# Kernel tuning notes

Hardware: AMD Instinct MI355X
Metric: run time of the kernel (lower is better)

Reference implementation:

```python
import jax, jax.numpy as jnp
import numpy as np

D = 256        # emb_dim
H = 16         # num_heads
HD = D // H    # head_dim
N = 16384      # num users
B, S = 64, 128 # seq batch / length; M = B*S


def setup_inputs() -> dict:
    key = jax.random.key(0)
    ks = jax.random.split(key, 8)
    scale = 1.0 / np.sqrt(D)
    return {
        "user_feat": jax.random.normal(ks[0], (N, D), dtype=jnp.float32),
        "seq_feat": jax.random.normal(ks[1], (B, S, D), dtype=jnp.float32),
        "in_proj_w": jax.random.uniform(ks[2], (3 * D, D), jnp.float32, -scale, scale),
        "in_proj_b": jnp.zeros((3 * D,), jnp.float32),
        "out_proj_w": jax.random.uniform(ks[3], (D, D), jnp.float32, -scale, scale),
        "out_proj_b": jnp.zeros((D,), jnp.float32),
        "trans_w": jax.random.uniform(ks[4], (D, D), jnp.float32, -scale, scale),
        "trans_b": jax.random.uniform(ks[5], (D,), jnp.float32, -scale, scale),
    }


def _mha(x, in_proj_w, in_proj_b, out_proj_w, out_proj_b):
    # x: [B, S, D] self-attention, batch_first, like nn.MultiheadAttention
    qkv = jnp.einsum("bsd,ed->bse", x, in_proj_w) + in_proj_b  # [B,S,3D]
    q, k, v = jnp.split(qkv, 3, axis=-1)
    def heads(t):  # [B,S,D] -> [B,H,S,HD]
        return t.reshape(B, S, H, HD).transpose(0, 2, 1, 3)
    q, k, v = heads(q), heads(k), heads(v)
    scores = jnp.einsum("bhqd,bhkd->bhqk", q, k) / np.sqrt(HD)
    attn = jax.nn.softmax(scores, axis=-1)
    out = jnp.einsum("bhqk,bhkd->bhqd", attn, v)  # [B,H,S,HD]
    out = out.transpose(0, 2, 1, 3).reshape(B, S, D)
    return out @ out_proj_w.T + out_proj_b


def reference(user_feat, seq_feat, in_proj_w, in_proj_b, out_proj_w, out_proj_b, trans_w, trans_b):
    seq = _mha(seq_feat, in_proj_w, in_proj_b, out_proj_w, out_proj_b)
    seq = seq.reshape(-1, D)                        # [M, D]
    M = seq.shape[0]
    att = user_feat @ seq.T                         # [N, M]
    att = att / jnp.maximum(jnp.sum(jnp.abs(att), axis=1, keepdims=True), 1e-12)  # F.normalize p=1
    # mean_j Linear(att_ij * seq_j) == Linear((att @ seq) / M)  (exact, by linearity)
    agg = (att @ seq) / M                           # [N, D]
    return user_feat + (agg @ trans_w.T + trans_b)
```

## Files before the change

kernel.cpp:

```cpp
#include <hip/hip_runtime.h>


typedef __bf16 bf16_t;
typedef __bf16 bf16x8 __attribute__((ext_vector_type(8)));
typedef __bf16 bf16x4 __attribute__((ext_vector_type(4)));
typedef float  f32x4  __attribute__((ext_vector_type(4)));
typedef unsigned int u32x4 __attribute__((ext_vector_type(4)));

#define MFMA16(a, b, c) __builtin_amdgcn_mfma_f32_16x16x32_bf16((a), (b), (c), 0, 0, 0)

#define AS1 __attribute__((address_space(1)))
#define AS3 __attribute__((address_space(3)))
#define GLOAD_LDS16(g, l) \
    __builtin_amdgcn_global_load_lds((const AS1 unsigned int*)(const void*)(g), \
                                     (AS3 unsigned int*)(void*)(l), 16, 0, 0)

__device__ __forceinline__ int swz256(int row, int k) { return row * 256 + (k ^ ((row & 7) << 3)); }

__global__ void k_cvt(const float* __restrict__ s, bf16_t* __restrict__ d, int n4) {
    int i  = blockIdx.x * blockDim.x + threadIdx.x;
    int st = gridDim.x * blockDim.x;
    for (; i < n4; i += st) {
        float4 v = ((const float4*)s)[i];
        bf16x4 o = { (bf16_t)v.x, (bf16_t)v.y, (bf16_t)v.z, (bf16_t)v.w };
        ((bf16x4*)d)[i] = o;
    }
}

__global__ __launch_bounds__(256, 1)
void k_gemm_bt(const bf16_t* __restrict__ A, const bf16_t* __restrict__ B,
               const float* __restrict__ bias, bf16_t* __restrict__ Cb, int N) {
    __shared__ bf16_t Al[64 * 256];
    __shared__ bf16_t Bl[64 * 256];
    const int tid  = threadIdx.x;
    const int lane = tid & 63;
    const int w    = tid >> 6;
    const int l15  = lane & 15;
    const int l4   = lane >> 4;
    const int rb = blockIdx.y * 64, cb = blockIdx.x * 64;

    {
        const u32x4* sa = (const u32x4*)(A + (size_t)rb * 256);
        const u32x4* sb = (const u32x4*)(B + (size_t)cb * 256);
        u32x4* da = (u32x4*)Al;
        u32x4* db = (u32x4*)Bl;
#pragma unroll
        for (int i = 0; i < 8; ++i) {
            int ch  = i * 256 + tid;
            int row = ch >> 5, cp = ch & 31;
            int sch = (ch & ~31) | (cp ^ (row & 7));
            da[sch] = sa[ch];
            db[sch] = sb[ch];
        }
    }
    __syncthreads();

    f32x4 acc[4];
#pragma unroll
    for (int n = 0; n < 4; ++n) acc[n] = (f32x4){0.f, 0.f, 0.f, 0.f};
#pragma unroll
    for (int t = 0; t < 8; ++t) {
        int k = t * 32 + l4 * 8;
        bf16x8 af = *(const bf16x8*)(Al + swz256(16 * w + l15, k));
#pragma unroll
        for (int n = 0; n < 4; ++n) {
            bf16x8 bfr = *(const bf16x8*)(Bl + swz256(16 * n + l15, k));
            acc[n] = MFMA16(af, bfr, acc[n]);
        }
    }
#pragma unroll
    for (int n = 0; n < 4; ++n) {
        int col = cb + 16 * n + l15;
        float bv = bias ? bias[col] : 0.f;
#pragma unroll
        for (int r = 0; r < 4; ++r) {
            int row = rb + 16 * w + l4 * 4 + r;
            Cb[(size_t)row * N + col] = (bf16_t)(acc[n][r] + bv);
        }
    }
}

__global__ __launch_bounds__(256, 1)
void k_gemm_seqT(const bf16_t* __restrict__ A, const bf16_t* __restrict__ B,
                 const float* __restrict__ bias, bf16_t* __restrict__ Cb,
                 bf16_t* __restrict__ CTb) {
    __shared__ bf16_t Al[64 * 256];
    __shared__ bf16_t Bl[64 * 256];
    __shared__ float  Tt[64][65];
    const int tid  = threadIdx.x;
    const int lane = tid & 63;
    const int w    = tid >> 6;
    const int l15  = lane & 15;
    const int l4   = lane >> 4;
    const int rb = blockIdx.y * 64, cb = blockIdx.x * 64;

    {
        const u32x4* sa = (const u32x4*)(A + (size_t)rb * 256);
        const u32x4* sb = (const u32x4*)(B + (size_t)cb * 256);
        u32x4* da = (u32x4*)Al;
        u32x4* db = (u32x4*)Bl;
#pragma unroll
        for (int i = 0; i < 8; ++i) {
            int ch  = i * 256 + tid;
            int row = ch >> 5, cp = ch & 31;
            int sch = (ch & ~31) | (cp ^ (row & 7));
            da[sch] = sa[ch];
            db[sch] = sb[ch];
        }
    }
    __syncthreads();

    f32x4 acc[4];
#pragma unroll
    for (int n = 0; n < 4; ++n) acc[n] = (f32x4){0.f, 0.f, 0.f, 0.f};
#pragma unroll
    for (int t = 0; t < 8; ++t) {
        int k = t * 32 + l4 * 8;
        bf16x8 af = *(const bf16x8*)(Al + swz256(16 * w + l15, k));
#pragma unroll
        for (int n = 0; n < 4; ++n) {
            bf16x8 bfr = *(const bf16x8*)(Bl + swz256(16 * n + l15, k));
            acc[n] = MFMA16(af, bfr, acc[n]);
        }
    }
#pragma unroll
    for (int n = 0; n < 4; ++n) {
        int col = cb + 16 * n + l15;
        float bv = bias[col];
#pragma unroll
        for (int r = 0; r < 4; ++r) {
            int row = rb + 16 * w + l4 * 4 + r;
            float v = acc[n][r] + bv;
            Cb[(size_t)row * 256 + col] = (bf16_t)v;
            Tt[16 * n + l15][16 * w + l4 * 4 + r] = v;
        }
    }
    __syncthreads();
#pragma unroll
    for (int i = 0; i < 16; ++i) {
        int e = i * 256 + tid;
        int lc = e >> 6, lr = e & 63;
        CTb[(size_t)(cb + lc) * 8192 + rb + lr] = (bf16_t)Tt[lc][lr];
    }
}

__global__ __launch_bounds__(128, 1)
void k_mha(const bf16_t* __restrict__ qkv, bf16_t* __restrict__ attn) {
    __shared__ float Kl[128][17];
    __shared__ float Vl[128][17];
    const int bh = blockIdx.x;
    const int b = bh >> 4, h = bh & 15;
    const int t = threadIdx.x;
    const size_t rowbase = (size_t)b * 128;

    const bf16_t* base = qkv + (rowbase + t) * 768 + h * 16;
    bf16x8 qa = *(const bf16x8*)(base),       qb = *(const bf16x8*)(base + 8);
    bf16x8 ka = *(const bf16x8*)(base + 256), kb = *(const bf16x8*)(base + 264);
    bf16x8 va = *(const bf16x8*)(base + 512), vb = *(const bf16x8*)(base + 520);
    float q[16];
#pragma unroll
    for (int e = 0; e < 8; ++e) {
        q[e] = (float)qa[e]; q[8 + e] = (float)qb[e];
        Kl[t][e] = (float)ka[e]; Kl[t][8 + e] = (float)kb[e];
        Vl[t][e] = (float)va[e]; Vl[t][8 + e] = (float)vb[e];
    }
    __syncthreads();

    float m = -1e30f;
    for (int j = 0; j < 128; ++j) {
        float s = 0.f;
#pragma unroll
        for (int d = 0; d < 16; ++d) s += q[d] * Kl[j][d];
        m = fmaxf(m, s * 0.25f);
    }
    float sum = 0.f;
    float o[16];
#pragma unroll
    for (int d = 0; d < 16; ++d) o[d] = 0.f;
    for (int j = 0; j < 128; ++j) {
        float s = 0.f;
#pragma unroll
        for (int d = 0; d < 16; ++d) s += q[d] * Kl[j][d];
        float e = __expf(s * 0.25f - m);
        sum += e;
#pragma unroll
        for (int d = 0; d < 16; ++d) o[d] += e * Vl[j][d];
    }
    float inv = 1.f / sum;
    bf16_t* out = attn + (rowbase + t) * 256 + h * 16;
#pragma unroll
    for (int d = 0; d < 16; ++d) out[d] = (bf16_t)(o[d] * inv);
}

__global__ __launch_bounds__(512, 2)
void k_rowabs(const bf16_t* __restrict__ Ub, const bf16_t* __restrict__ Sq,
              float* __restrict__ rsp) {
    __shared__ bf16_t Kl[2][64 * 256];

    const int tid  = threadIdx.x;
    const int lane = tid & 63;
    const int wid  = tid >> 6;
    const int wr   = wid >> 2;
    const int wc   = wid & 3;
    const int l15  = lane & 15;
    const int l4   = lane >> 4;
    const int q0   = blockIdx.x * 128;
    const int jy   = blockIdx.y;
    const int jbase = jy * 4096;

    int koff[4];
#pragma unroll
    for (int i = 0; i < 4; ++i) {
        int c = wid * 256 + i * 64 + lane;
        int sc = (c & ~31) | ((c & 31) ^ ((c >> 5) & 7));
        koff[i] = sc * 16;
    }
    auto stage = [&](int b, int j0) {
        const char* gK = (const char*)Sq + (size_t)j0 * 512;
        char* lK = (char*)(&Kl[b][0]) + wid * 4096;
#pragma unroll
        for (int i = 0; i < 4; ++i) GLOAD_LDS16(gK + koff[i], lK + i * 1024);
    };

    bf16x8 uf[4][8];
#pragma unroll
    for (int rt = 0; rt < 4; ++rt) {
        const bf16_t* up = Ub + (size_t)(q0 + 64 * wr + 16 * rt + l15) * 256 + l4 * 8;
#pragma unroll
        for (int t = 0; t < 8; ++t) uf[rt][t] = *(const bf16x8*)(up + t * 32);
    }

    float rsacc[4][4];
#pragma unroll
    for (int rt = 0; rt < 4; ++rt)
#pragma unroll
        for (int r = 0; r < 4; ++r) rsacc[rt][r] = 0.f;

    stage(0, jbase);
    __syncthreads();

    for (int it = 0; it < 64; ++it) {
        const int cur = it & 1;
        if (it + 1 < 64) stage(cur ^ 1, jbase + (it + 1) * 64);
        const bf16_t* Klc = &Kl[cur][0];

        f32x4 sacc[4];
#pragma unroll
        for (int rt = 0; rt < 4; ++rt) sacc[rt] = (f32x4){0.f, 0.f, 0.f, 0.f};
#pragma unroll
        for (int t = 0; t < 8; ++t) {
            int k = t * 32 + l4 * 8;
            bf16x8 bfr = *(const bf16x8*)(Klc + swz256(16 * wc + l15, k));
#pragma unroll
            for (int rt = 0; rt < 4; ++rt)
                sacc[rt] = MFMA16(uf[rt][t], bfr, sacc[rt]);
        }
#pragma unroll
        for (int rt = 0; rt < 4; ++rt)
#pragma unroll
            for (int r = 0; r < 4; ++r) rsacc[rt][r] += fabsf(sacc[rt][r]);
        __syncthreads();
    }

    float* rdst = rsp + (size_t)(jy * 4 + wc) * 16384 + q0 + 64 * wr;
#pragma unroll
    for (int rt = 0; rt < 4; ++rt)
#pragma unroll
        for (int r = 0; r < 4; ++r) {
            float v = rsacc[rt][r];
            v += __shfl_xor(v, 1, 16);
            v += __shfl_xor(v, 2, 16);
            v += __shfl_xor(v, 4, 16);
            v += __shfl_xor(v, 8, 16);
            if (l15 == 0) rdst[16 * rt + 4 * l4 + r] = v;
        }
}

__global__ void k_rs(const float* __restrict__ rsp, float* __restrict__ rs) {
    int i = blockIdx.x * blockDim.x + threadIdx.x;
    float s = 0.f;
#pragma unroll
    for (int p = 0; p < 8; ++p) s += rsp[(size_t)p * 16384 + i];
    rs[i] = 1.f / (fmaxf(s, 1e-12f) * 8192.f);
}

__global__ __launch_bounds__(256, 1)
void k_gram(const bf16_t* __restrict__ ST, float* __restrict__ Gpart) {
    __shared__ bf16_t Al[64 * 256];
    __shared__ bf16_t Bl[64 * 256];
    const int tid = threadIdx.x, lane = tid & 63, w = tid >> 6;
    const int l15 = lane & 15, l4 = lane >> 4;
    const int rb = blockIdx.y * 64, cb = blockIdx.x * 64;
    const int jb = blockIdx.z * 1024;

    f32x4 acc[4];
#pragma unroll
    for (int n = 0; n < 4; ++n) acc[n] = (f32x4){0.f, 0.f, 0.f, 0.f};

    for (int kt4 = 0; kt4 < 4; ++kt4) {
        int j0 = jb + kt4 * 256;
        __syncthreads();
        u32x4* da = (u32x4*)Al;
        u32x4* db = (u32x4*)Bl;
#pragma unroll
        for (int i = 0; i < 8; ++i) {
            int ch  = i * 256 + tid;
            int row = ch >> 5, cp = ch & 31;
            int sch = (ch & ~31) | (cp ^ (row & 7));
            da[sch] = *(const u32x4*)(ST + (size_t)(rb + row) * 8192 + j0 + cp * 8);
            db[sch] = *(const u32x4*)(ST + (size_t)(cb + row) * 8192 + j0 + cp * 8);
        }
        __syncthreads();
#pragma unroll
        for (int t = 0; t < 8; ++t) {
            int k = t * 32 + l4 * 8;
            bf16x8 af = *(const bf16x8*)(Al + swz256(16 * w + l15, k));
#pragma unroll
            for (int n = 0; n < 4; ++n) {
                bf16x8 bfr = *(const bf16x8*)(Bl + swz256(16 * n + l15, k));
                acc[n] = MFMA16(af, bfr, acc[n]);
            }
        }
    }
    float* gp = Gpart + (size_t)blockIdx.z * 65536;
#pragma unroll
    for (int n = 0; n < 4; ++n)
#pragma unroll
        for (int r = 0; r < 4; ++r)
            gp[(size_t)(rb + 16 * w + l4 * 4 + r) * 256 + cb + 16 * n + l15] = acc[n][r];
}

__global__ __launch_bounds__(256, 1)
void k_gh(const float* __restrict__ Gpart, const float* __restrict__ W,
          bf16_t* __restrict__ HT) {
    __shared__ bf16_t Al[64 * 256];
    __shared__ bf16_t Bl[64 * 256];
    const int tid = threadIdx.x, lane = tid & 63, w = tid >> 6;
    const int l15 = lane & 15, l4 = lane >> 4;
    const int rb = blockIdx.y * 64, cb = blockIdx.x * 64;

#pragma unroll
    for (int i = 0; i < 16; ++i) {
        int idx = i * 1024 + tid * 4;
        int row = idx >> 8, col = idx & 255;
        f32x4 s = *(const f32x4*)(Gpart + (size_t)(rb + row) * 256 + col);
#pragma unroll
        for (int p = 1; p < 8; ++p)
            s += *(const f32x4*)(Gpart + (size_t)p * 65536 + (size_t)(rb + row) * 256 + col);
        f32x4 wv = *(const f32x4*)(W + (size_t)(cb + row) * 256 + col);
        int sc = col ^ ((row & 7) << 3);
        bf16x4 ga = { (bf16_t)s[0], (bf16_t)s[1], (bf16_t)s[2], (bf16_t)s[3] };
        bf16x4 wb = { (bf16_t)wv[0], (bf16_t)wv[1], (bf16_t)wv[2], (bf16_t)wv[3] };
        *(bf16x4*)(Al + row * 256 + sc) = ga;
        *(bf16x4*)(Bl + row * 256 + sc) = wb;
    }
    __syncthreads();

    f32x4 acc[4];
#pragma unroll
    for (int n = 0; n < 4; ++n) acc[n] = (f32x4){0.f, 0.f, 0.f, 0.f};
#pragma unroll
    for (int t = 0; t < 8; ++t) {
        int k = t * 32 + l4 * 8;
        bf16x8 af = *(const bf16x8*)(Al + swz256(16 * w + l15, k));
#pragma unroll
        for (int n = 0; n < 4; ++n) {
            bf16x8 bfr = *(const bf16x8*)(Bl + swz256(16 * n + l15, k));
            acc[n] = MFMA16(af, bfr, acc[n]);
        }
    }
#pragma unroll
    for (int n = 0; n < 4; ++n)
#pragma unroll
        for (int r = 0; r < 4; ++r)
            HT[(size_t)(cb + 16 * n + l15) * 256 + rb + 16 * w + l4 * 4 + r] =
                (bf16_t)acc[n][r];
}

__global__ __launch_bounds__(256, 1)
void k_final(const bf16_t* __restrict__ A, const bf16_t* __restrict__ B,
             const float* __restrict__ rs, const float* __restrict__ tb,
             const float* __restrict__ user, float* __restrict__ out) {
    __shared__ bf16_t Al[64 * 256];
    __shared__ bf16_t Bl[64 * 256];
    const int tid  = threadIdx.x;
    const int lane = tid & 63;
    const int w    = tid >> 6;
    const int l15  = lane & 15;
    const int l4   = lane >> 4;
    const int rb = blockIdx.y * 64, cb = blockIdx.x * 64;

    {
        const u32x4* sa = (const u32x4*)(A + (size_t)rb * 256);
        const u32x4* sb = (const u32x4*)(B + (size_t)cb * 256);
        u32x4* da = (u32x4*)Al;
        u32x4* db = (u32x4*)Bl;
#pragma unroll
        for (int i = 0; i < 8; ++i) {
            int ch  = i * 256 + tid;
            int row = ch >> 5, cp = ch & 31;
            int sch = (ch & ~31) | (cp ^ (row & 7));
            da[sch] = sa[ch];
            db[sch] = sb[ch];
        }
    }
    __syncthreads();

    f32x4 acc[4];
#pragma unroll
    for (int n = 0; n < 4; ++n) acc[n] = (f32x4){0.f, 0.f, 0.f, 0.f};
#pragma unroll
    for (int t = 0; t < 8; ++t) {
        int k = t * 32 + l4 * 8;
        bf16x8 af = *(const bf16x8*)(Al + swz256(16 * w + l15, k));
#pragma unroll
        for (int n = 0; n < 4; ++n) {
            bf16x8 bfr = *(const bf16x8*)(Bl + swz256(16 * n + l15, k));
            acc[n] = MFMA16(af, bfr, acc[n]);
        }
    }
    float c[4];
#pragma unroll
    for (int r = 0; r < 4; ++r) c[r] = rs[rb + 16 * w + l4 * 4 + r];
#pragma unroll
    for (int n = 0; n < 4; ++n) {
        int col = cb + 16 * n + l15;
        float bv = tb[col];
#pragma unroll
        for (int r = 0; r < 4; ++r) {
            int row = rb + 16 * w + l4 * 4 + r;
            size_t idx = (size_t)row * 256 + col;
            out[idx] = user[idx] + c[r] * acc[n][r] + bv;
        }
    }
}

extern "C" void kernel_launch(void* const* d_in, const int* in_sizes, int n_in,
                              void* d_out, int out_size, void* d_ws, size_t ws_size,
                              hipStream_t stream) {
    const float* user_feat  = (const float*)d_in[0];
    const float* seq_feat   = (const float*)d_in[1];
    const float* in_proj_w  = (const float*)d_in[2];
    const float* in_proj_b  = (const float*)d_in[3];
    const float* out_proj_w = (const float*)d_in[4];
    const float* out_proj_b = (const float*)d_in[5];
    const float* trans_w    = (const float*)d_in[6];
    const float* trans_b    = (const float*)d_in[7];
    float* out = (float*)d_out;

    char* w = (char*)d_ws;
    size_t off = 0;
    auto take = [&](size_t bytes) { void* p = w + off; off += (bytes + 255) & ~(size_t)255; return p; };
    bf16_t* Ub    = (bf16_t*)take((size_t)16384 * 256 * 2);
    bf16_t* Xb    = (bf16_t*)take((size_t)8192 * 256 * 2);
    bf16_t* W1b   = (bf16_t*)take((size_t)768 * 256 * 2);
    bf16_t* W2b   = (bf16_t*)take((size_t)256 * 256 * 2);
    bf16_t* attnb = (bf16_t*)take((size_t)8192 * 256 * 2);
    bf16_t* seqb  = (bf16_t*)take((size_t)8192 * 256 * 2);
    bf16_t* seqTb = (bf16_t*)take((size_t)256 * 8192 * 2);
    char*   regA  = (char*)take((size_t)8192 * 768 * 4);
    bf16_t* qkvb  = (bf16_t*)regA;
    float*  Gpart = (float*)regA;
    bf16_t* HTb   = (bf16_t*)(regA + (size_t)8 * 65536 * 4);
    float*  rsp   = (float*)Xb;
    float*  rs    = (float*)(Xb + (size_t)8 * 16384 * 2);

    k_cvt<<<2048, 256, 0, stream>>>(user_feat, Ub, 16384 * 256 / 4);
    k_cvt<<<2048, 256, 0, stream>>>(seq_feat, Xb, 8192 * 256 / 4);
    k_cvt<<<192, 256, 0, stream>>>(in_proj_w, W1b, 768 * 256 / 4);
    k_cvt<<<64, 256, 0, stream>>>(out_proj_w, W2b, 256 * 256 / 4);

    k_gemm_bt<<<dim3(12, 128), 256, 0, stream>>>(Xb, W1b, in_proj_b, qkvb, 768);

    k_mha<<<1024, 128, 0, stream>>>(qkvb, attnb);

    k_gemm_seqT<<<dim3(4, 128), 256, 0, stream>>>(attnb, W2b, out_proj_b, seqb, seqTb);

    k_rowabs<<<dim3(128, 2), 512, 0, stream>>>(Ub, seqb, rsp);
    k_rs<<<64, 256, 0, stream>>>(rsp, rs);

    k_gram<<<dim3(4, 4, 8), 256, 0, stream>>>(seqTb, Gpart);
    k_gh<<<dim3(4, 4), 256, 0, stream>>>(Gpart, trans_w, HTb);

    k_final<<<dim3(4, 256), 256, 0, stream>>>(Ub, HTb, rs, trans_b, user_feat, out);
}
```

Baseline: 183.7 us.

## Fuse conversions into consumers, merge cvt launches, triple-buffer rowabs staging

Drops the standalone user_feat bf16 conversion and converts fp32 user rows on the fly inside k_rowabs and k_final. The remaining three conversions are merged into one launch, and the k_rs reduction is folded into k_final via shared memory. k_rowabs moves to a 3-stage LDS ring with explicit vmcnt waits and a single barrier per iteration, replacing double buffering with two syncs. The aim is less memory traffic and fewer launches, at the cost of reading fp32 user data twice and running k_rowabs at occupancy 1 with more LDS.

```diff
diff --git a/kernel.cpp b/kernel.cpp
--- a/kernel.cpp
+++ b/kernel.cpp
@@ -17,13 +17,22 @@
 
 __device__ __forceinline__ int swz256(int row, int k) { return row * 256 + (k ^ ((row & 7) << 3)); }
 
-__global__ void k_cvt(const float* __restrict__ s, bf16_t* __restrict__ d, int n4) {
+__global__ void k_cvt_all(const float* __restrict__ x, const float* __restrict__ w1,
+                          const float* __restrict__ w2,
+                          bf16_t* __restrict__ xb, bf16_t* __restrict__ w1b,
+                          bf16_t* __restrict__ w2b) {
+    const int NX = 8192 * 256 / 4, NW1 = 768 * 256 / 4, NW2 = 256 * 256 / 4;
+    const int total = NX + NW1 + NW2;
     int i  = blockIdx.x * blockDim.x + threadIdx.x;
     int st = gridDim.x * blockDim.x;
-    for (; i < n4; i += st) {
-        float4 v = ((const float4*)s)[i];
+    for (; i < total; i += st) {
+        const float* s; bf16_t* d; int k;
+        if (i < NX)            { s = x;  d = xb;  k = i; }
+        else if (i < NX + NW1) { s = w1; d = w1b; k = i - NX; }
+        else                   { s = w2; d = w2b; k = i - NX - NW1; }
+        float4 v = ((const float4*)s)[k];
         bf16x4 o = { (bf16_t)v.x, (bf16_t)v.y, (bf16_t)v.z, (bf16_t)v.w };
-        ((bf16x4*)d)[i] = o;
+        ((bf16x4*)d)[k] = o;
     }
 }
 
@@ -192,10 +201,10 @@
     for (int d = 0; d < 16; ++d) out[d] = (bf16_t)(o[d] * inv);
 }
 
-__global__ __launch_bounds__(512, 2)
-void k_rowabs(const bf16_t* __restrict__ Ub, const bf16_t* __restrict__ Sq,
+__global__ __launch_bounds__(512, 1)
+void k_rowabs(const float* __restrict__ Uf, const bf16_t* __restrict__ Sq,
               float* __restrict__ rsp) {
-    __shared__ bf16_t Kl[2][64 * 256];
+    __shared__ bf16_t Kl[3][64 * 256];
 
     const int tid  = threadIdx.x;
     const int lane = tid & 63;
@@ -207,6 +216,7 @@
     const int q0   = blockIdx.x * 128;
     const int jy   = blockIdx.y;
     const int jbase = jy * 4096;
+    const int NT   = 64;
 
     int koff[4];
 #pragma unroll
@@ -225,9 +235,15 @@
     bf16x8 uf[4][8];
 #pragma unroll
     for (int rt = 0; rt < 4; ++rt) {
-        const bf16_t* up = Ub + (size_t)(q0 + 64 * wr + 16 * rt + l15) * 256 + l4 * 8;
-#pragma unroll
-        for (int t = 0; t < 8; ++t) uf[rt][t] = *(const bf16x8*)(up + t * 32);
+        const float* up = Uf + (size_t)(q0 + 64 * wr + 16 * rt + l15) * 256 + l4 * 8;
+#pragma unroll
+        for (int t = 0; t < 8; ++t) {
+            float4 fa = *(const float4*)(up + t * 32);
+            float4 fb = *(const float4*)(up + t * 32 + 4);
+            bf16x8 v = { (bf16_t)fa.x, (bf16_t)fa.y, (bf16_t)fa.z, (bf16_t)fa.w,
+                         (bf16_t)fb.x, (bf16_t)fb.y, (bf16_t)fb.z, (bf16_t)fb.w };
+            uf[rt][t] = v;
+        }
     }
 
     float rsacc[4][4];
@@ -237,13 +253,20 @@
         for (int r = 0; r < 4; ++r) rsacc[rt][r] = 0.f;
 
     stage(0, jbase);
-    __syncthreads();
-
-    for (int it = 0; it < 64; ++it) {
-        const int cur = it & 1;
-        if (it + 1 < 64) stage(cur ^ 1, jbase + (it + 1) * 64);
+    stage(1, jbase + 64);
+
+    int cur = 0;
+    for (int it = 0; it < NT; ++it) {
+        if (it + 1 < NT) asm volatile("s_waitcnt vmcnt(4)" ::: "memory");
+        else             asm volatile("s_waitcnt vmcnt(0)" ::: "memory");
+        __builtin_amdgcn_s_barrier();
+        __builtin_amdgcn_sched_barrier(0);
+        if (it + 2 < NT) {
+            int nb = cur + 2; if (nb >= 3) nb -= 3;
+            stage(nb, jbase + (it + 2) * 64);
+        }
+
         const bf16_t* Klc = &Kl[cur][0];
-
         f32x4 sacc[4];
 #pragma unroll
         for (int rt = 0; rt < 4; ++rt) sacc[rt] = (f32x4){0.f, 0.f, 0.f, 0.f};
@@ -259,7 +282,8 @@
         for (int rt = 0; rt < 4; ++rt)
 #pragma unroll
             for (int r = 0; r < 4; ++r) rsacc[rt][r] += fabsf(sacc[rt][r]);
-        __syncthreads();
+
+        ++cur; if (cur >= 3) cur = 0;
     }
 
     float* rdst = rsp + (size_t)(jy * 4 + wc) * 16384 + q0 + 64 * wr;
@@ -274,14 +298,6 @@
             v += __shfl_xor(v, 8, 16);
             if (l15 == 0) rdst[16 * rt + 4 * l4 + r] = v;
         }
-}
-
-__global__ void k_rs(const float* __restrict__ rsp, float* __restrict__ rs) {
-    int i = blockIdx.x * blockDim.x + threadIdx.x;
-    float s = 0.f;
-#pragma unroll
-    for (int p = 0; p < 8; ++p) s += rsp[(size_t)p * 16384 + i];
-    rs[i] = 1.f / (fmaxf(s, 1e-12f) * 8192.f);
 }
 
 __global__ __launch_bounds__(256, 1)
@@ -378,11 +394,12 @@
 }
 
 __global__ __launch_bounds__(256, 1)
-void k_final(const bf16_t* __restrict__ A, const bf16_t* __restrict__ B,
-             const float* __restrict__ rs, const float* __restrict__ tb,
-             const float* __restrict__ user, float* __restrict__ out) {
+void k_final(const float* __restrict__ user, const bf16_t* __restrict__ B,
+             const float* __restrict__ rsp, const float* __restrict__ tb,
+             float* __restrict__ out) {
     __shared__ bf16_t Al[64 * 256];
     __shared__ bf16_t Bl[64 * 256];
+    __shared__ float  crs[64];
     const int tid  = threadIdx.x;
     const int lane = tid & 63;
     const int w    = tid >> 6;
@@ -391,18 +408,27 @@
     const int rb = blockIdx.y * 64, cb = blockIdx.x * 64;
 
     {
-        const u32x4* sa = (const u32x4*)(A + (size_t)rb * 256);
         const u32x4* sb = (const u32x4*)(B + (size_t)cb * 256);
-        u32x4* da = (u32x4*)Al;
         u32x4* db = (u32x4*)Bl;
 #pragma unroll
         for (int i = 0; i < 8; ++i) {
             int ch  = i * 256 + tid;
             int row = ch >> 5, cp = ch & 31;
             int sch = (ch & ~31) | (cp ^ (row & 7));
-            da[sch] = sa[ch];
+            const float* up = user + (size_t)(rb + row) * 256 + cp * 8;
+            float4 fa = *(const float4*)up;
+            float4 fb = *(const float4*)(up + 4);
+            bf16x8 v = { (bf16_t)fa.x, (bf16_t)fa.y, (bf16_t)fa.z, (bf16_t)fa.w,
+                         (bf16_t)fb.x, (bf16_t)fb.y, (bf16_t)fb.z, (bf16_t)fb.w };
+            *(bf16x8*)(Al + sch * 8) = v;
             db[sch] = sb[ch];
         }
+    }
+    if (tid < 64) {
+        float s = 0.f;
+#pragma unroll
+        for (int p = 0; p < 8; ++p) s += rsp[(size_t)p * 16384 + rb + tid];
+        crs[tid] = 1.f / (fmaxf(s, 1e-12f) * 8192.f);
     }
     __syncthreads();
 
@@ -421,7 +447,7 @@
     }
     float c[4];
 #pragma unroll
-    for (int r = 0; r < 4; ++r) c[r] = rs[rb + 16 * w + l4 * 4 + r];
+    for (int r = 0; r < 4; ++r) c[r] = crs[16 * w + l4 * 4 + r];
 #pragma unroll
     for (int n = 0; n < 4; ++n) {
         int col = cb + 16 * n + l15;
@@ -451,7 +477,6 @@
     char* w = (char*)d_ws;
     size_t off = 0;
     auto take = [&](size_t bytes) { void* p = w + off; off += (bytes + 255) & ~(size_t)255; return p; };
-    bf16_t* Ub    = (bf16_t*)take((size_t)16384 * 256 * 2);
     bf16_t* Xb    = (bf16_t*)take((size_t)8192 * 256 * 2);
     bf16_t* W1b   = (bf16_t*)take((size_t)768 * 256 * 2);
     bf16_t* W2b   = (bf16_t*)take((size_t)256 * 256 * 2);
@@ -463,12 +488,8 @@
     float*  Gpart = (float*)regA;
     bf16_t* HTb   = (bf16_t*)(regA + (size_t)8 * 65536 * 4);
     float*  rsp   = (float*)Xb;
-    float*  rs    = (float*)(Xb + (size_t)8 * 16384 * 2);
-
-    k_cvt<<<2048, 256, 0, stream>>>(user_feat, Ub, 16384 * 256 / 4);
-    k_cvt<<<2048, 256, 0, stream>>>(seq_feat, Xb, 8192 * 256 / 4);
-    k_cvt<<<192, 256, 0, stream>>>(in_proj_w, W1b, 768 * 256 / 4);
-    k_cvt<<<64, 256, 0, stream>>>(out_proj_w, W2b, 256 * 256 / 4);
+
+    k_cvt_all<<<1024, 256, 0, stream>>>(seq_feat, in_proj_w, out_proj_w, Xb, W1b, W2b);
 
     k_gemm_bt<<<dim3(12, 128), 256, 0, stream>>>(Xb, W1b, in_proj_b, qkvb, 768);
 
@@ -476,11 +497,10 @@
 
     k_gemm_seqT<<<dim3(4, 128), 256, 0, stream>>>(attnb, W2b, out_proj_b, seqb, seqTb);
 
-    k_rowabs<<<dim3(128, 2), 512, 0, stream>>>(Ub, seqb, rsp);
-    k_rs<<<64, 256, 0, stream>>>(rsp, rs);
+    k_rowabs<<<dim3(128, 2), 512, 0, stream>>>(user_feat, seqb, rsp);
 
     k_gram<<<dim3(4, 4, 8), 256, 0, stream>>>(seqTb, Gpart);
     k_gh<<<dim3(4, 4), 256, 0, stream>>>(Gpart, trans_w, HTb);
 
-    k_final<<<dim3(4, 256), 256, 0, stream>>>(Ub, HTb, rs, trans_b, user_feat, out);
-}
+    k_final<<<dim3(4, 256), 256, 0, stream>>>(user_feat, HTb, rsp, trans_b, out);
+}
```

New measurement: 188.1 us. 2.4% more time.
